# Optimization experiments

Hardware: AMD Instinct MI355X
Metric: run time of the kernel (lower is better)

The kernel has to match this reference:

```python
import jax, jax.numpy as jnp
import numpy as np

N_BONDS = 50000
N_EDGES = 600000
BOND_DIM = 64
SPH_DIM = 64
UNITS = 64


def setup_inputs() -> dict:
    key = jax.random.key(0)
    k1, k2, k3, k4, k5 = jax.random.split(key, 5)
    bond_features = jax.random.normal(k1, (N_BONDS, BOND_DIM), dtype=jnp.float32)
    edges_sph_features = jax.random.normal(k2, (N_EDGES, SPH_DIM), dtype=jnp.float32)
    # column 0: sorted segment ids (tf.math.segment_sum requires sorted ids)
    seg = jnp.sort(jax.random.randint(k3, (N_EDGES,), 0, N_BONDS, dtype=jnp.int32))
    nbr = jax.random.randint(k4, (N_EDGES,), 0, N_BONDS, dtype=jnp.int32)
    edges_neighbor = jnp.stack([seg, nbr], axis=1)  # [n_edges, 2]
    kernel = jax.random.normal(k5, (BOND_DIM + SPH_DIM, UNITS), dtype=jnp.float32) * 0.05
    bias = jnp.zeros((UNITS,), dtype=jnp.float32)
    return {
        "bond_features": bond_features,
        "edges_sph_features": edges_sph_features,
        "edges_neighbor": edges_neighbor,
        "kernel": kernel,
        "bias": bias,
    }


def reference(bond_features, edges_sph_features, edges_neighbor, kernel, bias):
    # gather bond features of the neighboring bond for each edge (line-graph)
    gathered = bond_features[edges_neighbor[:, 1]]            # [E, bond_dim]
    concated = jnp.concatenate([gathered, edges_sph_features], axis=-1)  # [E, bond_dim+sph_dim]
    # scatter-reduce into segments (sorted ids; fixed num_segments for jit)
    aggregated = jax.ops.segment_sum(
        concated, edges_neighbor[:, 0], num_segments=N_BONDS,
        indices_are_sorted=True,
    )  # [n_bonds, bond_dim+sph_dim]
    return aggregated @ kernel + bias
```

## Files before the change

### kernel.cpp

```cpp
#include <hip/hip_runtime.h>

#define N_BONDS 50000
#define N_EDGES 600000
#define R_BONDS 4
#define THREADS 512
#define BONDS_PER_BLOCK 32

typedef float f4 __attribute__((ext_vector_type(4)));

__device__ __forceinline__ float bcastf(float v, int l) {
    return __builtin_bit_cast(float, __builtin_amdgcn_readlane(__builtin_bit_cast(int, v), l));
}
__device__ __forceinline__ f4 f4zero() { return (f4){0.f, 0.f, 0.f, 0.f}; }
__device__ __forceinline__ void fma4(f4& a, float s, const f4& b) {
    a.x = fmaf(s, b.x, a.x); a.y = fmaf(s, b.y, a.y);
    a.z = fmaf(s, b.z, a.z); a.w = fmaf(s, b.w, a.w);
}

__global__ __launch_bounds__(256)
void fill_starts(const int* __restrict__ edges, int* __restrict__ starts) {
    const int e = blockIdx.x * blockDim.x + threadIdx.x;
    if (e >= N_EDGES) return;
    const int2* edges2 = (const int2*)edges;
    const int s  = edges2[e].x;
    const int sp = (e == 0) ? -1 : edges2[e - 1].x;
    for (int b = sp + 1; b <= s; ++b) starts[b] = e;
    if (e == N_EDGES - 1)
        for (int b = s + 1; b <= N_BONDS; ++b) starts[b] = N_EDGES;
}

__global__ __launch_bounds__(THREADS, 4)
void fused_gather_segsum_mm(const float* __restrict__ bond,
                            const float* __restrict__ sph,
                            const int*   __restrict__ edges,
                            const float* __restrict__ Kmat,
                            const float* __restrict__ bias,
                            const int*   __restrict__ starts,
                            float* __restrict__ out)
{
    __shared__ float ldsK[128 * 64];
    const int tid  = threadIdx.x;
    const int lane = tid & 63;
    const int wid  = tid >> 6;
    const int fl   = lane & 15;
    const int sg   = lane >> 4;

    {
        const f4* K4 = (const f4*)Kmat;
        f4*       L4 = (f4*)ldsK;
        #pragma unroll
        for (int i = 0; i < 4; ++i) L4[tid + i * THREADS] = K4[tid + i * THREADS];
    }
    __syncthreads();

    const int b0 = blockIdx.x * BONDS_PER_BLOCK + wid * R_BONDS;
    if (b0 >= N_BONDS) return;

    int st[R_BONDS + 1];
    #pragma unroll
    for (int r = 0; r <= R_BONDS; ++r)
        st[r] = __builtin_amdgcn_readfirstlane(starts[b0 + r]);

    const int eb    = st[0];
    const int total = st[R_BONDS] - eb;

    const f4*   bond4  = (const f4*)bond;
    const f4*   sph4   = (const f4*)sph;
    const int2* edges2 = (const int2*)edges;

    float slotG[R_BONDS], slotS[R_BONDS];
    f4 aG = f4zero(), aS = f4zero();
    int r = 0, cs = 0, bnd = st[1] - eb;

    auto txr = [&](f4 v) -> float {
        v.x += __shfl_xor(v.x, 16); v.y += __shfl_xor(v.y, 16);
        v.z += __shfl_xor(v.z, 16); v.w += __shfl_xor(v.w, 16);
        v.x += __shfl_xor(v.x, 32); v.y += __shfl_xor(v.y, 32);
        v.z += __shfl_xor(v.z, 32); v.w += __shfl_xor(v.w, 32);
        const int src = lane >> 2;
        const float s0 = __shfl(v.x, src), s1 = __shfl(v.y, src);
        const float s2 = __shfl(v.z, src), s3 = __shfl(v.w, src);
        const float r01 = (lane & 1) ? s1 : s0;
        const float r23 = (lane & 1) ? s3 : s2;
        return (lane & 2) ? r23 : r01;
    };

    auto slowpath = [&](int q, f4 GV, f4 SV) {
        const int qe = q + sg;
        while (true) {
            const float m = (qe >= cs && qe < bnd) ? 1.f : 0.f;
            fma4(aG, m, GV); fma4(aS, m, SV);
            if (bnd > q + 4) break;
            const float tG = txr(aG), tS = txr(aS);
            #pragma unroll
            for (int rr = 0; rr < R_BONDS; ++rr)
                if (rr == r) { slotG[rr] = tG; slotS[rr] = tS; }
            aG = f4zero(); aS = f4zero();
            cs = bnd;
            ++r;
            if (r >= R_BONDS) { bnd = 0x7fffffff; break; }
            #pragma unroll
            for (int rr = 2; rr <= R_BONDS; ++rr)
                if (r + 1 == rr) bnd = st[rr] - eb;
        }
    };

    int w0 = 0;
    while (w0 < total) {
        int wlen = total - w0; if (wlen > 64) wlen = 64;
        int2 p = make_int2(0, 0);
        if (lane < wlen) p = edges2[eb + w0 + lane];
        const int ng = (wlen + 3) >> 2;

        f4 gA, sA, gB, sB, gC, sC, gD, sD;

#define ISS(QQ, GV, SV) do { \
        if ((QQ) < ng) { \
            const int idx_ = (QQ) * 4 + sg; \
            const int nbr_ = __shfl(p.y, idx_); \
            int qe_ = w0 + idx_; if (qe_ >= total) qe_ = total - 1; \
            GV = bond4[nbr_ * 16 + fl]; \
            SV = sph4[(eb + qe_) * 16 + fl]; \
        } else { GV = f4zero(); SV = f4zero(); } } while (0)

#define ACC(QQ, GV, SV) do { \
        const int q_ = w0 + (QQ) * 4; \
        if (q_ + 4 <= bnd) { aG += GV; aS += SV; } \
        else slowpath(q_, GV, SV); } while (0)

        ISS(0, gA, sA); ISS(1, gB, sB); ISS(2, gC, sC); ISS(3, gD, sD);
        int q = 0;
        for (; q + 4 <= ng; q += 4) {
            ACC(q + 0, gA, sA); ISS(q + 4, gA, sA);
            ACC(q + 1, gB, sB); ISS(q + 5, gB, sB);
            ACC(q + 2, gC, sC); ISS(q + 6, gC, sC);
            ACC(q + 3, gD, sD); ISS(q + 7, gD, sD);
        }
        if (q + 0 < ng) ACC(q + 0, gA, sA);
        if (q + 1 < ng) ACC(q + 1, gB, sB);
        if (q + 2 < ng) ACC(q + 2, gC, sC);
#undef ISS
#undef ACC
        w0 += wlen;
    }

    {
        const float tG = txr(aG), tS = txr(aS);
        #pragma unroll
        for (int rr = 0; rr < R_BONDS; ++rr) {
            if (rr == r)     { slotG[rr] = tG;  slotS[rr] = tS; }
            else if (rr > r) { slotG[rr] = 0.f; slotS[rr] = 0.f; }
        }
    }

    float acc[R_BONDS];
    const float bl = bias[lane];
    #pragma unroll
    for (int rr = 0; rr < R_BONDS; ++rr) acc[rr] = bl;

    #pragma unroll 4
    for (int d = 0; d < 64; ++d) {
        const float kt = ldsK[d * 64 + lane];
        const float kb = ldsK[(64 + d) * 64 + lane];
        #pragma unroll
        for (int rr = 0; rr < R_BONDS; ++rr) {
            acc[rr] = fmaf(bcastf(slotG[rr], d), kt, acc[rr]);
            acc[rr] = fmaf(bcastf(slotS[rr], d), kb, acc[rr]);
        }
    }

    #pragma unroll
    for (int rr = 0; rr < R_BONDS; ++rr)
        if (b0 + rr < N_BONDS)
            __builtin_nontemporal_store(acc[rr], &out[(b0 + rr) * 64 + lane]);
}

extern "C" void kernel_launch(void* const* d_in, const int* in_sizes, int n_in,
                              void* d_out, int out_size, void* d_ws, size_t ws_size,
                              hipStream_t stream) {
    const float* bond  = (const float*)d_in[0];
    const float* sph   = (const float*)d_in[1];
    const int*   edges = (const int*)d_in[2];
    const float* Kmat  = (const float*)d_in[3];
    const float* bias  = (const float*)d_in[4];
    float* out  = (float*)d_out;
    int* starts = (int*)d_ws;

    fill_starts<<<(N_EDGES + 255) / 256, 256, 0, stream>>>(edges, starts);

    const int nblocks = (N_BONDS + BONDS_PER_BLOCK - 1) / BONDS_PER_BLOCK;
    fused_gather_segsum_mm<<<nblocks, THREADS, 0, stream>>>(bond, sph, edges, Kmat,
                                                            bias, starts, out);
}
```

Before: 74.22 us.

## Premultiply bond features by kernel into bf16 table before gather

Adds a prep kernel that computes bond_features @ K_top once per bond and stores it as bf16. The main kernel then gathers and sums these bf16 rows directly, so its dense matmul only covers the sph half. This halves the bytes of the random neighbor gather and removes half the per-bond matmul work. The cost is an extra pass over the bond table and bf16 rounding error in the gathered half.

```diff
diff --git a/kernel.cpp b/kernel.cpp
--- a/kernel.cpp
+++ b/kernel.cpp
@@ -5,8 +5,11 @@
 #define R_BONDS 4
 #define THREADS 512
 #define BONDS_PER_BLOCK 32
+#define STARTS_BLOCKS ((N_EDGES + 255) / 256)
+#define PREMUL_BLOCKS ((N_BONDS + 31) / 32)
 
 typedef float f4 __attribute__((ext_vector_type(4)));
+typedef unsigned short u16x4 __attribute__((ext_vector_type(4)));
 
 __device__ __forceinline__ float bcastf(float v, int l) {
     return __builtin_bit_cast(float, __builtin_amdgcn_readlane(__builtin_bit_cast(int, v), l));
@@ -16,21 +19,71 @@
     a.x = fmaf(s, b.x, a.x); a.y = fmaf(s, b.y, a.y);
     a.z = fmaf(s, b.z, a.z); a.w = fmaf(s, b.w, a.w);
 }
+__device__ __forceinline__ float bf2f(unsigned short u) {
+    return __builtin_bit_cast(float, ((unsigned)u) << 16);
+}
+__device__ __forceinline__ unsigned short f2bf(float f) {
+    unsigned u = __builtin_bit_cast(unsigned, f);
+    return (unsigned short)((u + 0x7fffu + ((u >> 16) & 1u)) >> 16);
+}
+__device__ __forceinline__ f4 cvt4(u16x4 u) {
+    return (f4){bf2f(u.x), bf2f(u.y), bf2f(u.z), bf2f(u.w)};
+}
 
 __global__ __launch_bounds__(256)
-void fill_starts(const int* __restrict__ edges, int* __restrict__ starts) {
-    const int e = blockIdx.x * blockDim.x + threadIdx.x;
-    if (e >= N_EDGES) return;
-    const int2* edges2 = (const int2*)edges;
-    const int s  = edges2[e].x;
-    const int sp = (e == 0) ? -1 : edges2[e - 1].x;
-    for (int b = sp + 1; b <= s; ++b) starts[b] = e;
-    if (e == N_EDGES - 1)
-        for (int b = s + 1; b <= N_BONDS; ++b) starts[b] = N_EDGES;
+void prep(const int* __restrict__ edges, int* __restrict__ starts,
+          const float* __restrict__ bond, const float* __restrict__ Kmat,
+          unsigned short* __restrict__ bondKb) {
+    __shared__ float ldsK[64 * 64];
+    const int tid = threadIdx.x;
+
+    if (blockIdx.x < STARTS_BLOCKS) {
+        const int e = blockIdx.x * 256 + tid;
+        if (e >= N_EDGES) return;
+        const int2* edges2 = (const int2*)edges;
+        const int s  = edges2[e].x;
+        const int sp = (e == 0) ? -1 : edges2[e - 1].x;
+        for (int b = sp + 1; b <= s; ++b) starts[b] = e;
+        if (e == N_EDGES - 1)
+            for (int b = s + 1; b <= N_BONDS; ++b) starts[b] = N_EDGES;
+        return;
+    }
+
+    const int bid  = blockIdx.x - STARTS_BLOCKS;
+    const int lane = tid & 63;
+    const int wid  = tid >> 6;
+    {
+        const f4* K4 = (const f4*)Kmat;
+        f4* L4 = (f4*)ldsK;
+        #pragma unroll
+        for (int i = 0; i < 4; ++i) L4[tid + i * 256] = K4[tid + i * 256];
+    }
+    __syncthreads();
+    const int row0 = bid * 32 + wid * 8;
+    if (row0 >= N_BONDS) return;
+
+    float rowv[8], acc[8];
+    #pragma unroll
+    for (int r = 0; r < 8; ++r) {
+        int ri = row0 + r; if (ri >= N_BONDS) ri = N_BONDS - 1;
+        rowv[r] = bond[ri * 64 + lane];
+        acc[r]  = 0.f;
+    }
+    #pragma unroll 4
+    for (int d = 0; d < 64; ++d) {
+        const float k = ldsK[d * 64 + lane];
+        #pragma unroll
+        for (int r = 0; r < 8; ++r)
+            acc[r] = fmaf(bcastf(rowv[r], d), k, acc[r]);
+    }
+    #pragma unroll
+    for (int r = 0; r < 8; ++r)
+        if (row0 + r < N_BONDS)
+            bondKb[(row0 + r) * 64 + lane] = f2bf(acc[r]);
 }
 
 __global__ __launch_bounds__(THREADS, 4)
-void fused_gather_segsum_mm(const float* __restrict__ bond,
+void fused_gather_segsum_mm(const unsigned short* __restrict__ bondKb,
                             const float* __restrict__ sph,
                             const int*   __restrict__ edges,
                             const float* __restrict__ Kmat,
@@ -38,7 +91,7 @@
                             const int*   __restrict__ starts,
                             float* __restrict__ out)
 {
-    __shared__ float ldsK[128 * 64];
+    __shared__ float ldsK[64 * 64];
     const int tid  = threadIdx.x;
     const int lane = tid & 63;
     const int wid  = tid >> 6;
@@ -49,7 +102,7 @@
         const f4* K4 = (const f4*)Kmat;
         f4*       L4 = (f4*)ldsK;
         #pragma unroll
-        for (int i = 0; i < 4; ++i) L4[tid + i * THREADS] = K4[tid + i * THREADS];
+        for (int i = 0; i < 2; ++i) L4[tid + i * THREADS] = K4[1024 + tid + i * THREADS];
     }
     __syncthreads();
 
@@ -64,9 +117,9 @@
     const int eb    = st[0];
     const int total = st[R_BONDS] - eb;
 
-    const f4*   bond4  = (const f4*)bond;
-    const f4*   sph4   = (const f4*)sph;
-    const int2* edges2 = (const int2*)edges;
+    const u16x4* bk4    = (const u16x4*)bondKb;
+    const f4*    sph4   = (const f4*)sph;
+    const int2*  edges2 = (const int2*)edges;
 
     float slotG[R_BONDS], slotS[R_BONDS];
     f4 aG = f4zero(), aS = f4zero();
@@ -112,33 +165,35 @@
         if (lane < wlen) p = edges2[eb + w0 + lane];
         const int ng = (wlen + 3) >> 2;
 
-        f4 gA, sA, gB, sB, gC, sC, gD, sD;
-
-#define ISS(QQ, GV, SV) do { \
+        u16x4 uA, uB, uC, uD;
+        f4 sA, sB, sC, sD;
+
+#define ISS(QQ, UV, SV) do { \
         if ((QQ) < ng) { \
             const int idx_ = (QQ) * 4 + sg; \
             const int nbr_ = __shfl(p.y, idx_); \
             int qe_ = w0 + idx_; if (qe_ >= total) qe_ = total - 1; \
-            GV = bond4[nbr_ * 16 + fl]; \
+            UV = bk4[nbr_ * 16 + fl]; \
             SV = sph4[(eb + qe_) * 16 + fl]; \
-        } else { GV = f4zero(); SV = f4zero(); } } while (0)
-
-#define ACC(QQ, GV, SV) do { \
+        } else { UV = (u16x4){0,0,0,0}; SV = f4zero(); } } while (0)
+
+#define ACC(QQ, UV, SV) do { \
         const int q_ = w0 + (QQ) * 4; \
-        if (q_ + 4 <= bnd) { aG += GV; aS += SV; } \
-        else slowpath(q_, GV, SV); } while (0)
-
-        ISS(0, gA, sA); ISS(1, gB, sB); ISS(2, gC, sC); ISS(3, gD, sD);
+        const f4 GVf = cvt4(UV); \
+        if (q_ + 4 <= bnd) { aG += GVf; aS += SV; } \
+        else slowpath(q_, GVf, SV); } while (0)
+
+        ISS(0, uA, sA); ISS(1, uB, sB); ISS(2, uC, sC); ISS(3, uD, sD);
         int q = 0;
         for (; q + 4 <= ng; q += 4) {
-            ACC(q + 0, gA, sA); ISS(q + 4, gA, sA);
-            ACC(q + 1, gB, sB); ISS(q + 5, gB, sB);
-            ACC(q + 2, gC, sC); ISS(q + 6, gC, sC);
-            ACC(q + 3, gD, sD); ISS(q + 7, gD, sD);
+            ACC(q + 0, uA, sA); ISS(q + 4, uA, sA);
+            ACC(q + 1, uB, sB); ISS(q + 5, uB, sB);
+            ACC(q + 2, uC, sC); ISS(q + 6, uC, sC);
+            ACC(q + 3, uD, sD); ISS(q + 7, uD, sD);
         }
-        if (q + 0 < ng) ACC(q + 0, gA, sA);
-        if (q + 1 < ng) ACC(q + 1, gB, sB);
-        if (q + 2 < ng) ACC(q + 2, gC, sC);
+        if (q + 0 < ng) ACC(q + 0, uA, sA);
+        if (q + 1 < ng) ACC(q + 1, uB, sB);
+        if (q + 2 < ng) ACC(q + 2, uC, sC);
 #undef ISS
 #undef ACC
         w0 += wlen;
@@ -156,17 +211,14 @@
     float acc[R_BONDS];
     const float bl = bias[lane];
     #pragma unroll
-    for (int rr = 0; rr < R_BONDS; ++rr) acc[rr] = bl;
+    for (int rr = 0; rr < R_BONDS; ++rr) acc[rr] = slotG[rr] + bl;
 
     #pragma unroll 4
     for (int d = 0; d < 64; ++d) {
-        const float kt = ldsK[d * 64 + lane];
-        const float kb = ldsK[(64 + d) * 64 + lane];
-        #pragma unroll
-        for (int rr = 0; rr < R_BONDS; ++rr) {
-            acc[rr] = fmaf(bcastf(slotG[rr], d), kt, acc[rr]);
+        const float kb = ldsK[d * 64 + lane];
+        #pragma unroll
+        for (int rr = 0; rr < R_BONDS; ++rr)
             acc[rr] = fmaf(bcastf(slotS[rr], d), kb, acc[rr]);
-        }
     }
 
     #pragma unroll
@@ -183,12 +235,15 @@
     const int*   edges = (const int*)d_in[2];
     const float* Kmat  = (const float*)d_in[3];
     const float* bias  = (const float*)d_in[4];
-    float* out  = (float*)d_out;
-    int* starts = (int*)d_ws;
-
-    fill_starts<<<(N_EDGES + 255) / 256, 256, 0, stream>>>(edges, starts);
+    float* out = (float*)d_out;
+
+    int*            starts = (int*)d_ws;
+    unsigned short* bondKb = (unsigned short*)((char*)d_ws + 262144);
+
+    prep<<<STARTS_BLOCKS + PREMUL_BLOCKS, 256, 0, stream>>>(edges, starts,
+                                                            bond, Kmat, bondKb);
 
     const int nblocks = (N_BONDS + BONDS_PER_BLOCK - 1) / BONDS_PER_BLOCK;
-    fused_gather_segsum_mm<<<nblocks, THREADS, 0, stream>>>(bond, sph, edges, Kmat,
+    fused_gather_segsum_mm<<<nblocks, THREADS, 0, stream>>>(bondKb, sph, edges, Kmat,
                                                             bias, starts, out);
 }
```

Result: slower. 75.84 us (+2.2%).
